# Kernel optimization log

Hardware: AMD Instinct MI355X
Metric: run time of the kernel (lower is better)

## Reference

```python
import jax, jax.numpy as jnp
import numpy as np

N = 50000      # nodes
E = 800000     # edges (before self loops)
F_IN = 128
HID = 32
HEADS = 4
C = 64         # num_classes
SLOPE = 0.2    # LeakyReLU negative slope (PyG GATConv default)


def setup_inputs() -> dict:
    key = jax.random.key(0)
    ks = jax.random.split(key, 16)
    def nrm(k, shape, scale=0.1):
        return jax.random.normal(k, shape, jnp.float32) * scale
    x = jax.random.normal(ks[0], (N, F_IN), jnp.float32)
    edge_index = jax.random.randint(ks[1], (2, E), 0, N, jnp.int32)
    # layer 1: F_IN -> HID per head, concat -> HEADS*HID
    w1 = nrm(ks[2], (F_IN, HEADS * HID)); as1 = nrm(ks[3], (HEADS, HID)); ad1 = nrm(ks[4], (HEADS, HID)); b1 = nrm(ks[5], (HEADS * HID,))
    # layer 2: HEADS*HID -> HID per head, concat
    w2 = nrm(ks[6], (HEADS * HID, HEADS * HID)); as2 = nrm(ks[7], (HEADS, HID)); ad2 = nrm(ks[8], (HEADS, HID)); b2 = nrm(ks[9], (HEADS * HID,))
    # layer 3: HEADS*HID -> C, single head, no concat (mean)
    w3 = nrm(ks[10], (HEADS * HID, C)); as3 = nrm(ks[11], (1, C)); ad3 = nrm(ks[12], (1, C)); b3 = nrm(ks[13], (C,))
    return {"x": x, "edge_index": edge_index,
            "w1": w1, "as1": as1, "ad1": ad1, "b1": b1,
            "w2": w2, "as2": as2, "ad2": ad2, "b2": b2,
            "w3": w3, "as3": as3, "ad3": ad3, "b3": b3}


def gat_conv(x, src, dst, W, a_src, a_dst, bias, heads, oc, concat):
    n = x.shape[0]
    h = (x @ W).reshape(n, heads, oc)                       # [N,H,F]
    al_s = jnp.einsum('nhf,hf->nh', h, a_src)               # [N,H]
    al_d = jnp.einsum('nhf,hf->nh', h, a_dst)
    e = jax.nn.leaky_relu(al_s[src] + al_d[dst], SLOPE)     # [E,H]
    # segment softmax over incoming edges per destination node
    m = jax.ops.segment_max(e, dst, num_segments=n)
    e = jnp.exp(e - m[dst])
    denom = jax.ops.segment_sum(e, dst, num_segments=n)
    alpha = e / denom[dst]                                  # [E,H]
    out = jax.ops.segment_sum(h[src] * alpha[:, :, None], dst, num_segments=n)  # [N,H,F]
    out = out.reshape(n, heads * oc) if concat else out.mean(axis=1)
    return out + bias


def reference(x, edge_index, w1, as1, ad1, b1, w2, as2, ad2, b2, w3, as3, ad3, b3):
    n = x.shape[0]
    loops = jnp.arange(n, dtype=edge_index.dtype)
    src = jnp.concatenate([edge_index[0], loops])           # add self loops (PyG default)
    dst = jnp.concatenate([edge_index[1], loops])
    h = gat_conv(x, src, dst, w1, as1, ad1, b1, HEADS, HID, True)
    h = jax.nn.relu(h)                                      # dropout is identity in eval
    h = gat_conv(h, src, dst, w2, as2, ad2, b2, HEADS, HID, True)
    h = jax.nn.relu(h)
    h = gat_conv(h, src, dst, w3, as3, ad3, b3, 1, C, False)
    return jax.nn.log_softmax(h, axis=1)
```

## Files before the change

### kernel.cpp

```cpp
#include <hip/hip_runtime.h>
#include <hip/hip_bf16.h>
#include <math.h>

#define SLOPE 0.2f
typedef unsigned int uint_t;
typedef unsigned short ushort_t;

static __device__ __forceinline__ float lrelu(float v) { return v > 0.f ? v : SLOPE * v; }
static __device__ __forceinline__ ushort_t f2b(float f) {
  uint_t u = __float_as_uint(f);
  u += 0x7fffu + ((u >> 16) & 1u);
  return (ushort_t)(u >> 16);
}
static __device__ __forceinline__ float2 b2x2(uint_t u) {
  union { uint_t u; __hip_bfloat162 b; } cv;
  cv.u = u;
  return __bfloat1622float2(cv.b);
}


__device__ __forceinline__ void hist_body(const int* __restrict__ ei, int* __restrict__ ts,
                                          int E, int N, int NB, int NBUCK, int b) {
  __shared__ int h[256];
  int tid = threadIdx.x;
  h[tid] = 0;
  __syncthreads();
  int ET = E + N;
  int base = b * 4096;
#pragma unroll
  for (int j = 0; j < 16; ++j) {
    int i = base + j * 256 + tid;
    if (i < ET) {
      int d = (i < E) ? ei[E + i] : (i - E);
      atomicAdd(&h[d >> 8], 1);
    }
  }
  __syncthreads();
  if (tid < NBUCK) ts[tid * NB + b] = h[tid];
}

__global__ __launch_bounds__(256) void scan1(int* __restrict__ a, int* __restrict__ bsum, int L) {
  int tid = threadIdx.x;
  int base = blockIdx.x * 1024 + tid * 4;
  int c0 = (base + 0 < L) ? a[base + 0] : 0;
  int c1 = (base + 1 < L) ? a[base + 1] : 0;
  int c2 = (base + 2 < L) ? a[base + 2] : 0;
  int c3 = (base + 3 < L) ? a[base + 3] : 0;
  int s = c0 + c1 + c2 + c3;
  int lane = tid & 63, wid = tid >> 6;
  int pre = s;
#pragma unroll
  for (int off = 1; off < 64; off <<= 1) {
    int t = __shfl_up(pre, off);
    if (lane >= off) pre += t;
  }
  __shared__ int wsum[4];
  if (lane == 63) wsum[wid] = pre;
  __syncthreads();
  int woff = 0;
#pragma unroll
  for (int w = 0; w < 4; ++w) woff += (w < wid) ? wsum[w] : 0;
  int excl = woff + pre - s;
  if (base + 0 < L) a[base + 0] = excl;
  if (base + 1 < L) a[base + 1] = excl + c0;
  if (base + 2 < L) a[base + 2] = excl + c0 + c1;
  if (base + 3 < L) a[base + 3] = excl + c0 + c1 + c2;
  if (tid == 255) bsum[blockIdx.x] = wsum[0] + wsum[1] + wsum[2] + wsum[3];
}

__global__ __launch_bounds__(1024) void scan2(int* __restrict__ bsum, int nb) {
  __shared__ int sh[1024];
  int tid = threadIdx.x;
  int v = (tid < nb) ? bsum[tid] : 0;
  sh[tid] = v;
  __syncthreads();
  for (int off = 1; off < 1024; off <<= 1) {
    int add = (tid >= off) ? sh[tid - off] : 0;
    __syncthreads();
    sh[tid] += add;
    __syncthreads();
  }
  if (tid < nb) bsum[tid] = sh[tid] - v;
}


__global__ __launch_bounds__(256) void part_kernel(const int* __restrict__ ei,
                                                   const int* __restrict__ ts,
                                                   const int* __restrict__ bsum,
                                                   uint_t* __restrict__ tmp,
                                                   int E, int N, int NB, int NBUCK) {
  __shared__ int bin[256];
  int tid = threadIdx.x, b = blockIdx.x;
  if (tid < NBUCK) {
    int idx = tid * NB + b;
    bin[tid] = ts[idx] + bsum[idx >> 10];
  }
  __syncthreads();
  int ET = E + N;
  int base = b * 4096;
#pragma unroll
  for (int j = 0; j < 16; ++j) {
    int i = base + j * 256 + tid;
    if (i < ET) {
      int s, d;
      if (i < E) { s = ei[i]; d = ei[E + i]; } else { s = i - E; d = i - E; }
      int pos = atomicAdd(&bin[d >> 8], 1);
      tmp[pos] = ((uint_t)d << 16) | (uint_t)s;
    }
  }
}

__global__ __launch_bounds__(256) void bucket_kernel(const uint_t* __restrict__ tmp,
                                                     const int* __restrict__ ts,
                                                     const int* __restrict__ bsum,
                                                     int* __restrict__ rowptr,
                                                     int* __restrict__ esrc,
                                                     int N, int NB, int NBUCK, int ET) {
  __shared__ int h[256], pref[256], rank[256];
  __shared__ int wsum[4];
  int tid = threadIdx.x, d = blockIdx.x;
  int i0 = d * NB;
  int start = ts[i0] + bsum[i0 >> 10];
  int end = ET;
  if (d != NBUCK - 1) {
    int i1 = (d + 1) * NB;
    end = ts[i1] + bsum[i1 >> 10];
  }
  h[tid] = 0; rank[tid] = 0;
  __syncthreads();
  for (int i = start + tid; i < end; i += 256)
    atomicAdd(&h[(tmp[i] >> 16) & 255], 1);
  __syncthreads();
  int v = h[tid];
  int lane = tid & 63, wid = tid >> 6;
  int inc = v;
#pragma unroll
  for (int off = 1; off < 64; off <<= 1) {
    int t = __shfl_up(inc, off);
    if (lane >= off) inc += t;
  }
  if (lane == 63) wsum[wid] = inc;
  __syncthreads();
  int woff = 0;
#pragma unroll
  for (int w = 0; w < 4; ++w) woff += (w < wid) ? wsum[w] : 0;
  pref[tid] = woff + inc - v;
  __syncthreads();
  int idx = d * 256 + tid;
  if (idx <= N) rowptr[idx] = start + pref[tid];
  for (int i = start + tid; i < end; i += 256) {
    uint_t v2 = tmp[i];
    int low = (v2 >> 16) & 255;
    int r = atomicAdd(&rank[low], 1);
    esrc[start + pref[low] + r] = (int)(v2 & 0xffffu);
  }
}


template<int OC, bool BF16IN>
__device__ __forceinline__ void gemm_body(const void* __restrict__ Xv,
                                          const float* __restrict__ W,
                                          ushort_t* __restrict__ H,
                                          const float* __restrict__ a_s,
                                          const float* __restrict__ a_d,
                                          float* __restrict__ als,
                                          float* __restrict__ ald,
                                          int N, int bid) {
  const int K = 128;
  const int CT = OC / 4;
  const int RPT = 64 / (256 / CT);
  __shared__ float xs[K][68];
  int tid = threadIdx.x;
  long row0 = (long)bid * 64;
  if (BF16IN) {
    const ushort_t* X = (const ushort_t*)Xv;
#pragma unroll
    for (int i = 0; i < 4; ++i) {
      int flat = i * 256 + tid;
      int r = flat & 63, kc = flat >> 6;
      long row = row0 + r;
      long rr = row < N ? row : (long)(N - 1);
      uint4 v = *(const uint4*)(X + rr * K + kc * 8);
      uint_t vv[4] = {v.x, v.y, v.z, v.w};
#pragma unroll
      for (int j = 0; j < 4; ++j) {
        float2 f = b2x2(vv[j]);
        xs[kc * 8 + j * 2 + 0][r] = f.x;
        xs[kc * 8 + j * 2 + 1][r] = f.y;
      }
    }
  } else {
    const float* X = (const float*)Xv;
#pragma unroll
    for (int i = 0; i < 8; ++i) {
      int flat = i * 256 + tid;
      int r = flat & 63, kc = flat >> 6;
      long row = row0 + r;
      long rr = row < N ? row : (long)(N - 1);
      float4 xv = *(const float4*)(X + rr * K + kc * 4);
      xs[kc * 4 + 0][r] = xv.x;
      xs[kc * 4 + 1][r] = xv.y;
      xs[kc * 4 + 2][r] = xv.z;
      xs[kc * 4 + 3][r] = xv.w;
    }
  }
  __syncthreads();
  int ct = tid % CT;
  int rg = tid / CT;
  int c0 = ct * 4;
  int r0 = rg * RPT;
  float acc[RPT][4];
#pragma unroll
  for (int i = 0; i < RPT; ++i)
    for (int j = 0; j < 4; ++j) acc[i][j] = 0.f;
#pragma unroll 4
  for (int k = 0; k < K; ++k) {
    float4 wv = *(const float4*)(W + (long)k * OC + c0);
    const float4* xr = (const float4*)(&xs[k][r0]);
#pragma unroll
    for (int i4 = 0; i4 < RPT / 4; ++i4) {
      float4 xv = xr[i4];
      float xa[4] = {xv.x, xv.y, xv.z, xv.w};
#pragma unroll
      for (int j = 0; j < 4; ++j) {
        int i = i4 * 4 + j;
        acc[i][0] = fmaf(xa[j], wv.x, acc[i][0]);
        acc[i][1] = fmaf(xa[j], wv.y, acc[i][1]);
        acc[i][2] = fmaf(xa[j], wv.z, acc[i][2]);
        acc[i][3] = fmaf(xa[j], wv.w, acc[i][3]);
      }
    }
  }
#pragma unroll
  for (int i = 0; i < RPT; ++i) {
    long row = row0 + r0 + i;
    if (row < N) {
      ushort4 o = {f2b(acc[i][0]), f2b(acc[i][1]), f2b(acc[i][2]), f2b(acc[i][3])};
      *(ushort4*)(H + row * OC + c0) = o;
    }
  }
  float4 sv = *(const float4*)(a_s + c0);
  float4 dv = *(const float4*)(a_d + c0);
  const int RED = (OC == 128) ? 4 : 8;
  const int GM  = (OC == 128) ? 7 : 15;
#pragma unroll
  for (int i = 0; i < RPT; ++i) {
    float ps = acc[i][0] * sv.x + acc[i][1] * sv.y + acc[i][2] * sv.z + acc[i][3] * sv.w;
    float pd = acc[i][0] * dv.x + acc[i][1] * dv.y + acc[i][2] * dv.z + acc[i][3] * dv.w;
#pragma unroll
    for (int off = 1; off <= RED; off <<= 1) {
      ps += __shfl_xor(ps, off);
      pd += __shfl_xor(pd, off);
    }
    long row = row0 + r0 + i;
    if ((ct & GM) == 0 && row < N) {
      if (OC == 128) {
        int head = c0 >> 5;
        als[row * 4 + head] = ps;
        ald[row * 4 + head] = pd;
      } else {
        als[row] = ps;
        ald[row] = pd;
      }
    }
  }
}

template<int OC, bool BF16IN>
__global__ __launch_bounds__(256) void gemm_tile(const void* __restrict__ Xv,
                                                 const float* __restrict__ W,
                                                 ushort_t* __restrict__ H,
                                                 const float* __restrict__ a_s,
                                                 const float* __restrict__ a_d,
                                                 float* __restrict__ als,
                                                 float* __restrict__ ald, int N) {
  gemm_body<OC, BF16IN>(Xv, W, H, a_s, a_d, als, ald, N, blockIdx.x);
}

__global__ __launch_bounds__(256) void k_gemm1_hist(const float* __restrict__ X,
    const float* __restrict__ W, ushort_t* __restrict__ H,
    const float* __restrict__ a_s, const float* __restrict__ a_d,
    float* __restrict__ als, float* __restrict__ ald, int N,
    const int* __restrict__ ei, int* __restrict__ ts, int E, int NB, int NBUCK,
    int gemmBlocks) {
  int bid = blockIdx.x;
  if (bid < gemmBlocks) gemm_body<128, false>(X, W, H, a_s, a_d, als, ald, N, bid);
  else hist_body(ei, ts, E, N, NB, NBUCK, bid - gemmBlocks);
}


__global__ __launch_bounds__(256) void gat_agg128(const ushort_t* __restrict__ h,
    const float* __restrict__ als, const float* __restrict__ ald,
    const int* __restrict__ rowptr, const int* __restrict__ esrc,
    const float* __restrict__ bias, ushort_t* __restrict__ out, int N) {
  int tid = threadIdx.x;
  int n = blockIdx.x * 8 + (tid >> 5);
  int l = tid & 31;
  int slot = l >> 3, sl = l & 7, hd = sl >> 1;
  if (n >= N) return;
  int beg = rowptr[n], end = rowptr[n + 1];
  float aldv = ald[(long)n * 4 + hd];
  float den = 0.f;
  float acc[16];
#pragma unroll
  for (int j = 0; j < 16; ++j) acc[j] = 0.f;
  for (int e = beg + slot; e < end; e += 4) {
    int s = esrc[e];
    float p = __expf(lrelu(als[(long)s * 4 + hd] + aldv));
    den += p;
    const ushort_t* hp = h + (long)s * 128 + sl * 16;
    uint4 v0 = *(const uint4*)(hp);
    uint4 v1 = *(const uint4*)(hp + 8);
    uint_t vv[8] = {v0.x, v0.y, v0.z, v0.w, v1.x, v1.y, v1.z, v1.w};
#pragma unroll
    for (int j = 0; j < 8; ++j) {
      float2 f = b2x2(vv[j]);
      acc[2 * j + 0] = fmaf(p, f.x, acc[2 * j + 0]);
      acc[2 * j + 1] = fmaf(p, f.y, acc[2 * j + 1]);
    }
  }
  den += __shfl_xor(den, 8); den += __shfl_xor(den, 16);
#pragma unroll
  for (int j = 0; j < 16; ++j) {
    acc[j] += __shfl_xor(acc[j], 8);
    acc[j] += __shfl_xor(acc[j], 16);
  }
  if (slot == 0) {
    float inv = 1.f / den;
    uint_t pk[8];
#pragma unroll
    for (int j = 0; j < 8; ++j) {
      float v0 = fmaxf(fmaf(acc[2 * j + 0], inv, bias[sl * 16 + 2 * j + 0]), 0.f);
      float v1 = fmaxf(fmaf(acc[2 * j + 1], inv, bias[sl * 16 + 2 * j + 1]), 0.f);
      pk[j] = (uint_t)f2b(v0) | ((uint_t)f2b(v1) << 16);
    }
    uint4 o0 = {pk[0], pk[1], pk[2], pk[3]};
    uint4 o1 = {pk[4], pk[5], pk[6], pk[7]};
    *(uint4*)(out + (long)n * 128 + sl * 16 + 0) = o0;
    *(uint4*)(out + (long)n * 128 + sl * 16 + 8) = o1;
  }
}

__global__ __launch_bounds__(256) void gat_agg64_lsm(const ushort_t* __restrict__ h,
    const float* __restrict__ als, const float* __restrict__ ald,
    const int* __restrict__ rowptr, const int* __restrict__ esrc,
    const float* __restrict__ bias, float* __restrict__ out, int N) {
  int tid = threadIdx.x;
  int n = blockIdx.x * 8 + (tid >> 5);
  int l = tid & 31;
  int slot = l >> 2, sl = l & 3;
  if (n >= N) return;
  int beg = rowptr[n], end = rowptr[n + 1];
  float aldv = ald[n];
  float den = 0.f;
  float acc[16];
#pragma unroll
  for (int j = 0; j < 16; ++j) acc[j] = 0.f;
  for (int e = beg + slot; e < end; e += 8) {
    int s = esrc[e];
    float p = __expf(lrelu(als[s] + aldv));
    den += p;
    const ushort_t* hp = h + (long)s * 64 + sl * 16;
    uint4 v0 = *(const uint4*)(hp);
    uint4 v1 = *(const uint4*)(hp + 8);
    uint_t vv[8] = {v0.x, v0.y, v0.z, v0.w, v1.x, v1.y, v1.z, v1.w};
#pragma unroll
    for (int j = 0; j < 8; ++j) {
      float2 f = b2x2(vv[j]);
      acc[2 * j + 0] = fmaf(p, f.x, acc[2 * j + 0]);
      acc[2 * j + 1] = fmaf(p, f.y, acc[2 * j + 1]);
    }
  }
  den += __shfl_xor(den, 4); den += __shfl_xor(den, 8); den += __shfl_xor(den, 16);
#pragma unroll
  for (int j = 0; j < 16; ++j) {
    acc[j] += __shfl_xor(acc[j], 4);
    acc[j] += __shfl_xor(acc[j], 8);
    acc[j] += __shfl_xor(acc[j], 16);
  }
  if (slot == 0) {
    float inv = 1.f / den;
    float v[16];
#pragma unroll
    for (int j = 0; j < 16; ++j) v[j] = fmaf(acc[j], inv, bias[sl * 16 + j]);
    float lm = v[0];
#pragma unroll
    for (int j = 1; j < 16; ++j) lm = fmaxf(lm, v[j]);
    lm = fmaxf(lm, __shfl_xor(lm, 1));
    lm = fmaxf(lm, __shfl_xor(lm, 2));
    float es = 0.f;
#pragma unroll
    for (int j = 0; j < 16; ++j) es += __expf(v[j] - lm);
    es += __shfl_xor(es, 1);
    es += __shfl_xor(es, 2);
    float lse = lm + __logf(es);
    float* op = out + (long)n * 64 + sl * 16;
#pragma unroll
    for (int q = 0; q < 4; ++q) {
      float4 o = {v[4 * q + 0] - lse, v[4 * q + 1] - lse, v[4 * q + 2] - lse, v[4 * q + 3] - lse};
      *(float4*)(op + 4 * q) = o;
    }
  }
}


extern "C" void kernel_launch(void* const* d_in, const int* in_sizes, int n_in,
                              void* d_out, int out_size, void* d_ws, size_t ws_size,
                              hipStream_t stream) {
  const float* x   = (const float*)d_in[0];
  const int*   ei  = (const int*)d_in[1];
  const float* w1  = (const float*)d_in[2];
  const float* as1 = (const float*)d_in[3];
  const float* ad1 = (const float*)d_in[4];
  const float* b1  = (const float*)d_in[5];
  const float* w2  = (const float*)d_in[6];
  const float* as2 = (const float*)d_in[7];
  const float* ad2 = (const float*)d_in[8];
  const float* b2  = (const float*)d_in[9];
  const float* w3  = (const float*)d_in[10];
  const float* as3 = (const float*)d_in[11];
  const float* ad3 = (const float*)d_in[12];
  const float* b3  = (const float*)d_in[13];
  float* out = (float*)d_out;

  const int N = in_sizes[0] / 128;
  const int E = in_sizes[1] / 2;
  const int ET = E + N;

  const int NB = (ET + 4095) / 4096;
  const int NBUCK = (N + 255) >> 8;
  const int SL = NBUCK * NB;
  const int nsb = (SL + 1023) / 1024;

  char* ws = (char*)d_ws;
  size_t off = 0;
  auto alloc = [&](size_t bytes) -> void* {
    void* p = ws + off;
    off += (bytes + 255) & ~(size_t)255;
    return p;
  };
  ushort_t* bufA = (ushort_t*)alloc((size_t)N * 128 * 2);
  ushort_t* bufB = (ushort_t*)alloc((size_t)N * 128 * 2);
  float* als   = (float*)alloc((size_t)N * 4 * 4);
  float* ald   = (float*)alloc((size_t)N * 4 * 4);
  int* ts      = (int*)alloc((size_t)SL * 4);
  int* bsum    = (int*)alloc((size_t)1024 * 4);
  uint_t* tmp  = (uint_t*)alloc((size_t)ET * 4);
  int* rowptr  = (int*)alloc((size_t)(N + 1) * 4);
  int* esrc    = (int*)alloc((size_t)ET * 4);

  const int ggrid = (N + 63) / 64;
  const int aggrid = (N + 7) / 8;

  k_gemm1_hist<<<ggrid + NB, 256, 0, stream>>>(x, w1, bufA, as1, ad1, als, ald, N,
                                               ei, ts, E, NB, NBUCK, ggrid);
  scan1<<<nsb, 256, 0, stream>>>(ts, bsum, SL);
  scan2<<<1, 1024, 0, stream>>>(bsum, nsb);
  part_kernel<<<NB, 256, 0, stream>>>(ei, ts, bsum, tmp, E, N, NB, NBUCK);
  bucket_kernel<<<NBUCK, 256, 0, stream>>>(tmp, ts, bsum, rowptr, esrc, N, NB, NBUCK, ET);

  gat_agg128<<<aggrid, 256, 0, stream>>>(bufA, als, ald, rowptr, esrc, b1, bufB, N);

  gemm_tile<128, true><<<ggrid, 256, 0, stream>>>(bufB, w2, bufA, as2, ad2, als, ald, N);
  gat_agg128<<<aggrid, 256, 0, stream>>>(bufA, als, ald, rowptr, esrc, b2, bufB, N);

  gemm_tile<64, true><<<ggrid, 256, 0, stream>>>(bufB, w3, bufA, as3, ad3, als, ald, N);
  gat_agg64_lsm<<<aggrid, 256, 0, stream>>>(bufA, als, ald, rowptr, esrc, b3, out, N);
}
```

Before: 298.5 us.

## Use bf16 MFMA for layer-2/3 GEMMs with pre-transposed bf16 weights

Replaces the FP32 FMA tiled GEMM for layers 2 and 3 with a kernel built on 16x16x32 bf16 MFMA instructions that reads bf16 activations straight into padded LDS. W2 and W3 are converted to bf16 and transposed by extra blocks in the first fused kernel, hiding that prep alongside the first GEMM and histogram. Attention logit dot products are computed from MFMA accumulators with cross-lane shuffles. This trades FP32 weight precision for bf16, which adds rounding error.

```diff
diff --git a/kernel.cpp b/kernel.cpp
--- a/kernel.cpp
+++ b/kernel.cpp
@@ -5,6 +5,8 @@
 #define SLOPE 0.2f
 typedef unsigned int uint_t;
 typedef unsigned short ushort_t;
+typedef __attribute__((ext_vector_type(8))) short short8;
+typedef __attribute__((ext_vector_type(4))) float f32x4;
 
 static __device__ __forceinline__ float lrelu(float v) { return v > 0.f ? v : SLOPE * v; }
 static __device__ __forceinline__ ushort_t f2b(float f) {
@@ -82,7 +84,6 @@
   }
   if (tid < nb) bsum[tid] = sh[tid] - v;
 }
-
 
 __global__ __launch_bounds__(256) void part_kernel(const int* __restrict__ ei,
                                                    const int* __restrict__ ts,
@@ -157,52 +158,32 @@
 }
 
 
-template<int OC, bool BF16IN>
-__device__ __forceinline__ void gemm_body(const void* __restrict__ Xv,
-                                          const float* __restrict__ W,
-                                          ushort_t* __restrict__ H,
-                                          const float* __restrict__ a_s,
-                                          const float* __restrict__ a_d,
-                                          float* __restrict__ als,
-                                          float* __restrict__ ald,
-                                          int N, int bid) {
+__device__ __forceinline__ void gemm1_body(const float* __restrict__ X,
+                                           const float* __restrict__ W,
+                                           ushort_t* __restrict__ H,
+                                           const float* __restrict__ a_s,
+                                           const float* __restrict__ a_d,
+                                           float* __restrict__ als,
+                                           float* __restrict__ ald,
+                                           int N, int bid) {
   const int K = 128;
-  const int CT = OC / 4;
-  const int RPT = 64 / (256 / CT);
+  const int OC = 128;
+  const int CT = 32;
+  const int RPT = 8;
   __shared__ float xs[K][68];
   int tid = threadIdx.x;
   long row0 = (long)bid * 64;
-  if (BF16IN) {
-    const ushort_t* X = (const ushort_t*)Xv;
-#pragma unroll
-    for (int i = 0; i < 4; ++i) {
-      int flat = i * 256 + tid;
-      int r = flat & 63, kc = flat >> 6;
-      long row = row0 + r;
-      long rr = row < N ? row : (long)(N - 1);
-      uint4 v = *(const uint4*)(X + rr * K + kc * 8);
-      uint_t vv[4] = {v.x, v.y, v.z, v.w};
-#pragma unroll
-      for (int j = 0; j < 4; ++j) {
-        float2 f = b2x2(vv[j]);
-        xs[kc * 8 + j * 2 + 0][r] = f.x;
-        xs[kc * 8 + j * 2 + 1][r] = f.y;
-      }
-    }
-  } else {
-    const float* X = (const float*)Xv;
-#pragma unroll
-    for (int i = 0; i < 8; ++i) {
-      int flat = i * 256 + tid;
-      int r = flat & 63, kc = flat >> 6;
-      long row = row0 + r;
-      long rr = row < N ? row : (long)(N - 1);
-      float4 xv = *(const float4*)(X + rr * K + kc * 4);
-      xs[kc * 4 + 0][r] = xv.x;
-      xs[kc * 4 + 1][r] = xv.y;
-      xs[kc * 4 + 2][r] = xv.z;
-      xs[kc * 4 + 3][r] = xv.w;
-    }
+#pragma unroll
+  for (int i = 0; i < 8; ++i) {
+    int flat = i * 256 + tid;
+    int r = flat & 63, kc = flat >> 6;
+    long row = row0 + r;
+    long rr = row < N ? row : (long)(N - 1);
+    float4 xv = *(const float4*)(X + rr * K + kc * 4);
+    xs[kc * 4 + 0][r] = xv.x;
+    xs[kc * 4 + 1][r] = xv.y;
+    xs[kc * 4 + 2][r] = xv.z;
+    xs[kc * 4 + 3][r] = xv.w;
   }
   __syncthreads();
   int ct = tid % CT;
@@ -241,40 +222,41 @@
   }
   float4 sv = *(const float4*)(a_s + c0);
   float4 dv = *(const float4*)(a_d + c0);
-  const int RED = (OC == 128) ? 4 : 8;
-  const int GM  = (OC == 128) ? 7 : 15;
 #pragma unroll
   for (int i = 0; i < RPT; ++i) {
     float ps = acc[i][0] * sv.x + acc[i][1] * sv.y + acc[i][2] * sv.z + acc[i][3] * sv.w;
     float pd = acc[i][0] * dv.x + acc[i][1] * dv.y + acc[i][2] * dv.z + acc[i][3] * dv.w;
 #pragma unroll
-    for (int off = 1; off <= RED; off <<= 1) {
+    for (int off = 1; off <= 4; off <<= 1) {
       ps += __shfl_xor(ps, off);
       pd += __shfl_xor(pd, off);
     }
     long row = row0 + r0 + i;
-    if ((ct & GM) == 0 && row < N) {
-      if (OC == 128) {
-        int head = c0 >> 5;
-        als[row * 4 + head] = ps;
-        ald[row * 4 + head] = pd;
-      } else {
-        als[row] = ps;
-        ald[row] = pd;
-      }
-    }
-  }
-}
-
-template<int OC, bool BF16IN>
-__global__ __launch_bounds__(256) void gemm_tile(const void* __restrict__ Xv,
-                                                 const float* __restrict__ W,
-                                                 ushort_t* __restrict__ H,
-                                                 const float* __restrict__ a_s,
-                                                 const float* __restrict__ a_d,
-                                                 float* __restrict__ als,
-                                                 float* __restrict__ ald, int N) {
-  gemm_body<OC, BF16IN>(Xv, W, H, a_s, a_d, als, ald, N, blockIdx.x);
+    if ((ct & 7) == 0 && row < N) {
+      int head = c0 >> 5;
+      als[row * 4 + head] = ps;
+      ald[row * 4 + head] = pd;
+    }
+  }
+}
+
+__device__ __forceinline__ void wprep_body(const float* __restrict__ w2,
+                                           const float* __restrict__ w3,
+                                           ushort_t* __restrict__ wt2,
+                                           ushort_t* __restrict__ wt3, int b) {
+  int tid = threadIdx.x;
+#pragma unroll
+  for (int j = 0; j < 32; ++j) {
+    int idx = b * 8192 + j * 256 + tid;
+    if (idx < 16384) {
+      int c = idx & 127, k = idx >> 7;
+      wt2[c * 128 + k] = f2b(w2[idx]);
+    } else if (idx < 24576) {
+      int i2 = idx - 16384;
+      int c = i2 & 63, k = i2 >> 6;
+      wt3[c * 128 + k] = f2b(w3[i2]);
+    }
+  }
 }
 
 __global__ __launch_bounds__(256) void k_gemm1_hist(const float* __restrict__ X,
@@ -282,10 +264,88 @@
     const float* __restrict__ a_s, const float* __restrict__ a_d,
     float* __restrict__ als, float* __restrict__ ald, int N,
     const int* __restrict__ ei, int* __restrict__ ts, int E, int NB, int NBUCK,
+    const float* __restrict__ w2, const float* __restrict__ w3,
+    ushort_t* __restrict__ wt2, ushort_t* __restrict__ wt3,
     int gemmBlocks) {
   int bid = blockIdx.x;
-  if (bid < gemmBlocks) gemm_body<128, false>(X, W, H, a_s, a_d, als, ald, N, bid);
-  else hist_body(ei, ts, E, N, NB, NBUCK, bid - gemmBlocks);
+  if (bid < gemmBlocks) gemm1_body(X, W, H, a_s, a_d, als, ald, N, bid);
+  else if (bid < gemmBlocks + NB) hist_body(ei, ts, E, N, NB, NBUCK, bid - gemmBlocks);
+  else wprep_body(w2, w3, wt2, wt3, bid - gemmBlocks - NB);
+}
+
+
+template<int OC>
+__global__ __launch_bounds__(256) void mfma_gemm(const ushort_t* __restrict__ X,
+    const ushort_t* __restrict__ WT, ushort_t* __restrict__ H,
+    const float* __restrict__ a_s, const float* __restrict__ a_d,
+    float* __restrict__ als, float* __restrict__ ald, int N) {
+  const int K = 128;
+  const int P = 136;
+  const int MT = OC / 16;
+  __shared__ ushort_t xs[64 * P];
+  int tid = threadIdx.x;
+  long row0 = (long)blockIdx.x * 64;
+#pragma unroll
+  for (int i = 0; i < 4; ++i) {
+    int flat = i * 256 + tid;
+    int r = flat & 63, kc = flat >> 6;
+    long row = row0 + r;
+    long rr = row < N ? row : (long)(N - 1);
+    uint4 v = *(const uint4*)(X + rr * K + kc * 8);
+    *(uint4*)(xs + r * P + kc * 8) = v;
+  }
+  __syncthreads();
+  int wave = tid >> 6, lane = tid & 63;
+  int n = lane & 15, q = lane >> 4;
+  int wrow = wave * 16 + n;
+  f32x4 acc[MT];
+#pragma unroll
+  for (int t = 0; t < MT; ++t) acc[t] = (f32x4){0.f, 0.f, 0.f, 0.f};
+#pragma unroll
+  for (int kk = 0; kk < 4; ++kk) {
+    short8 bfrag = *(const short8*)(xs + wrow * P + kk * 32 + q * 8);
+#pragma unroll
+    for (int t = 0; t < MT; ++t) {
+      short8 afrag = *(const short8*)(WT + (t * 16 + n) * K + kk * 32 + q * 8);
+      acc[t] = __builtin_amdgcn_mfma_f32_16x16x32_bf16(afrag, bfrag, acc[t], 0, 0, 0);
+    }
+  }
+  long grow = row0 + wrow;
+  bool valid = grow < N;
+  float ps[4] = {0.f, 0.f, 0.f, 0.f};
+  float pd[4] = {0.f, 0.f, 0.f, 0.f};
+#pragma unroll
+  for (int t = 0; t < MT; ++t) {
+    int fb = t * 16 + q * 4;
+    if (valid) {
+      uint_t lo = (uint_t)f2b(acc[t][0]) | ((uint_t)f2b(acc[t][1]) << 16);
+      uint_t hi = (uint_t)f2b(acc[t][2]) | ((uint_t)f2b(acc[t][3]) << 16);
+      uint2 pk = {lo, hi};
+      *(uint2*)(H + grow * OC + fb) = pk;
+    }
+    float4 sv = *(const float4*)(a_s + fb);
+    float4 dv = *(const float4*)(a_d + fb);
+    int hidx = (OC == 128) ? (t >> 1) : 0;
+    ps[hidx] += acc[t][0] * sv.x + acc[t][1] * sv.y + acc[t][2] * sv.z + acc[t][3] * sv.w;
+    pd[hidx] += acc[t][0] * dv.x + acc[t][1] * dv.y + acc[t][2] * dv.z + acc[t][3] * dv.w;
+  }
+  const int NH = (OC == 128) ? 4 : 1;
+#pragma unroll
+  for (int h = 0; h < NH; ++h) {
+    ps[h] += __shfl_xor(ps[h], 16); ps[h] += __shfl_xor(ps[h], 32);
+    pd[h] += __shfl_xor(pd[h], 16); pd[h] += __shfl_xor(pd[h], 32);
+  }
+  if (q == 0 && valid) {
+    if (OC == 128) {
+      float4 s4 = {ps[0], ps[1], ps[2], ps[3]};
+      float4 d4 = {pd[0], pd[1], pd[2], pd[3]};
+      *(float4*)(als + grow * 4) = s4;
+      *(float4*)(ald + grow * 4) = d4;
+    } else {
+      als[grow] = ps[0];
+      ald[grow] = pd[0];
+    }
+  }
 }
 
 
@@ -396,9 +456,9 @@
     float lse = lm + __logf(es);
     float* op = out + (long)n * 64 + sl * 16;
 #pragma unroll
-    for (int q = 0; q < 4; ++q) {
-      float4 o = {v[4 * q + 0] - lse, v[4 * q + 1] - lse, v[4 * q + 2] - lse, v[4 * q + 3] - lse};
-      *(float4*)(op + 4 * q) = o;
+    for (int qq = 0; qq < 4; ++qq) {
+      float4 o = {v[4 * qq + 0] - lse, v[4 * qq + 1] - lse, v[4 * qq + 2] - lse, v[4 * qq + 3] - lse};
+      *(float4*)(op + 4 * qq) = o;
     }
   }
 }
@@ -448,12 +508,15 @@
   uint_t* tmp  = (uint_t*)alloc((size_t)ET * 4);
   int* rowptr  = (int*)alloc((size_t)(N + 1) * 4);
   int* esrc    = (int*)alloc((size_t)ET * 4);
+  ushort_t* wt2 = (ushort_t*)alloc((size_t)128 * 128 * 2);
+  ushort_t* wt3 = (ushort_t*)alloc((size_t)64 * 128 * 2);
 
   const int ggrid = (N + 63) / 64;
   const int aggrid = (N + 7) / 8;
 
-  k_gemm1_hist<<<ggrid + NB, 256, 0, stream>>>(x, w1, bufA, as1, ad1, als, ald, N,
-                                               ei, ts, E, NB, NBUCK, ggrid);
+  k_gemm1_hist<<<ggrid + NB + 3, 256, 0, stream>>>(x, w1, bufA, as1, ad1, als, ald, N,
+                                                   ei, ts, E, NB, NBUCK,
+                                                   w2, w3, wt2, wt3, ggrid);
   scan1<<<nsb, 256, 0, stream>>>(ts, bsum, SL);
   scan2<<<1, 1024, 0, stream>>>(bsum, nsb);
   part_kernel<<<NB, 256, 0, stream>>>(ei, ts, bsum, tmp, E, N, NB, NBUCK);
@@ -461,9 +524,9 @@
 
   gat_agg128<<<aggrid, 256, 0, stream>>>(bufA, als, ald, rowptr, esrc, b1, bufB, N);
 
-  gemm_tile<128, true><<<ggrid, 256, 0, stream>>>(bufB, w2, bufA, as2, ad2, als, ald, N);
+  mfma_gemm<128><<<ggrid, 256, 0, stream>>>(bufB, wt2, bufA, as2, ad2, als, ald, N);
   gat_agg128<<<aggrid, 256, 0, stream>>>(bufA, als, ald, rowptr, esrc, b2, bufB, N);
 
-  gemm_tile<64, true><<<ggrid, 256, 0, stream>>>(bufB, w3, bufA, as3, ad3, als, ald, N);
+  mfma_gemm<64><<<ggrid, 256, 0, stream>>>(bufB, wt3, bufA, as3, ad3, als, ald, N);
   gat_agg64_lsm<<<aggrid, 256, 0, stream>>>(bufA, als, ald, rowptr, esrc, b3, out, N);
 }
```

After: 286.4 us. 4.1% less time.
